# Kernel tuning notes

Hardware: AMD Instinct MI355X
Metric: run time of the kernel (lower is better)

The kernel has to match this reference:

```python
import jax, jax.numpy as jnp
import numpy as np
import math

B, S, H, NH, NKV, HD = 1, 2048, 4096, 32, 8, 128
ROPE_THETA = 10000.0


def setup_inputs() -> dict:
    key = jax.random.key(0)
    ks = jax.random.split(key, 16)
    hidden_states = jax.random.normal(ks[0], (B, S, H), jnp.float32) * 0.02
    Wq = jax.random.normal(ks[1], (NH * HD, H), jnp.float32) * 0.02
    Wk = jax.random.normal(ks[2], (NKV * HD, H), jnp.float32) * 0.02
    Wv = jax.random.normal(ks[3], (NKV * HD, H), jnp.float32) * 0.02
    Wo = jax.random.normal(ks[4], (H, NH * HD), jnp.float32) * 0.02
    # RoPE cos/sin, HF Llama convention: emb = concat(freqs, freqs)
    inv_freq = 1.0 / (ROPE_THETA ** (jnp.arange(0, HD, 2, dtype=jnp.float32) / HD))
    pos = jnp.arange(S, dtype=jnp.float32)
    freqs = pos[:, None] * inv_freq[None, :]              # [S, HD/2]
    emb = jnp.concatenate([freqs, freqs], axis=-1)        # [S, HD]
    cos = jnp.cos(emb)[None]                              # [1, S, HD]
    sin = jnp.sin(emb)[None]
    # additive causal mask [B, 1, S, S]
    causal = jnp.tril(jnp.ones((S, S), dtype=bool))
    attention_mask = jnp.where(causal, 0.0, -1e9).astype(jnp.float32)[None, None]
    # reorder permutations (as written by GPTQ act-order reordering)
    perm = lambda k, n: jax.random.permutation(k, n).astype(jnp.int32)
    return {
        'hidden_states': hidden_states, 'Wq': Wq, 'Wk': Wk, 'Wv': Wv, 'Wo': Wo,
        'cos': cos, 'sin': sin, 'attention_mask': attention_mask,
        'q_order_col': perm(ks[5], H), 'q_order_row': perm(ks[6], NH * HD),
        'k_order_col': perm(ks[7], H), 'k_order_row': perm(ks[8], NKV * HD),
        'v_order_col': perm(ks[9], H), 'v_order_row': perm(ks[10], NKV * HD),
        'o_order_col': perm(ks[11], NH * HD), 'o_order_row': perm(ks[12], H),
    }


def _rotate_half(x):
    x1, x2 = jnp.split(x, 2, axis=-1)
    return jnp.concatenate([-x2, x1], axis=-1)


def reference(hidden_states, Wq, Wk, Wv, Wo, cos, sin, attention_mask,
              q_order_col, q_order_row, k_order_col, k_order_row,
              v_order_col, v_order_row, o_order_col, o_order_row):
    bsz, q_len, _ = hidden_states.shape
    # permuted projections: gather cols of input, GEMM, gather rows of output
    q = hidden_states[:, :, q_order_col] @ Wq.T
    q = q[:, :, q_order_row]
    k = hidden_states[:, :, k_order_col] @ Wk.T
    k = k[:, :, k_order_row]
    v = hidden_states[:, :, v_order_col] @ Wv.T
    v = v[:, :, v_order_row]
    q = q.reshape(bsz, q_len, NH, HD).transpose(0, 2, 1, 3)   # [B,NH,S,HD]
    k = k.reshape(bsz, q_len, NKV, HD).transpose(0, 2, 1, 3)  # [B,NKV,S,HD]
    v = v.reshape(bsz, q_len, NKV, HD).transpose(0, 2, 1, 3)
    # RoPE
    c = cos[:, None, :, :]  # [1,1,S,HD]
    s = sin[:, None, :, :]
    q = q * c + _rotate_half(q) * s
    k = k * c + _rotate_half(k) * s
    # repeat_kv for GQA
    rep = NH // NKV
    k = jnp.repeat(k, rep, axis=1)  # [B,NH,S,HD]
    v = jnp.repeat(v, rep, axis=1)
    # eager attention: full score matrix, fp32 softmax
    scores = jnp.einsum('bhqd,bhkd->bhqk', q, k) / math.sqrt(HD)
    scores = scores + attention_mask
    probs = jax.nn.softmax(scores.astype(jnp.float32), axis=-1).astype(q.dtype)
    # dropout p=0.0 (eval) -> identity
    attn = jnp.einsum('bhqk,bhkd->bhqd', probs, v)
    attn = attn.transpose(0, 2, 1, 3).reshape(bsz, q_len, NH * HD)
    out = attn[:, :, o_order_col] @ Wo.T
    out = out[:, :, o_order_row]
    return out
```

## Files before the change

kernel.cpp:

```cpp
#include <hip/hip_runtime.h>

typedef unsigned short u16;
typedef unsigned char u8;
typedef __bf16 bf16x8 __attribute__((ext_vector_type(8)));
typedef float f32x4 __attribute__((ext_vector_type(4)));
typedef int i32x4 __attribute__((ext_vector_type(4)));
typedef int i32x8 __attribute__((ext_vector_type(8)));

__device__ __forceinline__ u16 f2bf(float f) {
    unsigned u = __float_as_uint(f);
    unsigned r = (u + 0x7fffu + ((u >> 16) & 1u)) >> 16;
    return (u16)r;
}
__device__ __forceinline__ float bf2f(u16 h) {
    return __uint_as_float(((unsigned)h) << 16);
}
__device__ __forceinline__ unsigned pack_bf2(float lo, float hi) {
    unsigned a = __float_as_uint(hi) + 0x8000u;
    unsigned b = __float_as_uint(lo) + 0x8000u;
    return __builtin_amdgcn_perm(a, b, 0x07060302u);
}
__device__ __forceinline__ unsigned pack_fp8x4(float a, float b, float c, float d) {
    unsigned w = __builtin_amdgcn_cvt_pk_fp8_f32(a, b, 0, false);
    w = __builtin_amdgcn_cvt_pk_fp8_f32(c, d, w, true);
    return w;
}
__device__ __forceinline__ void async_copy16(const void* g, void* l) {
    __builtin_amdgcn_global_load_lds((__attribute__((address_space(1))) void*)(void*)g,
                                     (__attribute__((address_space(3))) void*)l, 16, 0, 0);
}

#define FP8_SCALE 64.0f
#define FP8_UNSCALE (1.0f / 4096.0f)


__global__ void inv4_k(const int* __restrict__ q, const int* __restrict__ k,
                       const int* __restrict__ v, const int* __restrict__ o,
                       int* __restrict__ invq, int* __restrict__ invk,
                       int* __restrict__ invv, int* __restrict__ invo) {
    int i = blockIdx.x * 256 + threadIdx.x;
    int a = i >> 12, j = i & 4095;
    const int* p = a == 0 ? q : a == 1 ? k : a == 2 ? v : o;
    int* inv = a == 0 ? invq : a == 1 ? invk : a == 2 ? invv : invo;
    inv[p[j]] = j;
}

__global__ __launch_bounds__(256) void permw4_k(
    const float* __restrict__ Wq, const float* __restrict__ Wk,
    const float* __restrict__ Wv, const float* __restrict__ Wo,
    const int* __restrict__ qor, const int* __restrict__ kor,
    const int* __restrict__ vor, const int* __restrict__ oor,
    const int* __restrict__ invq, const int* __restrict__ invk,
    const int* __restrict__ invv, const int* __restrict__ invo,
    u8* __restrict__ Wqkf8, u16* __restrict__ Wvp, u16* __restrict__ Wop) {
    __shared__ float rowbuf[4096];
    int j = blockIdx.x;
    const float* W; const int* rp; const int* inv; int row; int f8;
    u8* out8 = nullptr; u16* out16 = nullptr;
    if (j < 4096)      { W = Wq; rp = qor; inv = invq; row = j;        out8 = Wqkf8 + (size_t)j * 4096; f8 = 1; }
    else if (j < 5120) { W = Wk; rp = kor; inv = invk; row = j - 4096; out8 = Wqkf8 + (size_t)j * 4096; f8 = 1; }
    else if (j < 6144) { W = Wv; rp = vor; inv = invv; row = j - 5120; out16 = Wvp + (size_t)(j - 5120) * 4096; f8 = 0; }
    else               { W = Wo; rp = oor; inv = invo; row = j - 6144; out16 = Wop + (size_t)(j - 6144) * 4096; f8 = 0; }
    if (f8) {
        int hd = row & 127, b = hd >> 4;
        row = (row & ~127) | ((hd & 15) | ((b & 1) << 6) | ((b & 2) << 3) | ((hd & 64) >> 1));
    }
    const float4* wr4 = (const float4*)(W + (size_t)rp[row] * 4096);
#pragma unroll
    for (int t = 0; t < 4; t++)
        ((float4*)rowbuf)[threadIdx.x + t * 256] = wr4[threadIdx.x + t * 256];
    __syncthreads();
    if (f8) {
        int t = threadIdx.x;
        const int4* inv4p = (const int4*)inv;
        float v[16];
#pragma unroll
        for (int u = 0; u < 4; u++) {
            int4 ix = inv4p[t * 4 + u];
            v[4 * u + 0] = rowbuf[ix.x] * FP8_SCALE;
            v[4 * u + 1] = rowbuf[ix.y] * FP8_SCALE;
            v[4 * u + 2] = rowbuf[ix.z] * FP8_SCALE;
            v[4 * u + 3] = rowbuf[ix.w] * FP8_SCALE;
        }
        uint4 wv;
        wv.x = pack_fp8x4(v[0], v[1], v[2], v[3]);
        wv.y = pack_fp8x4(v[4], v[5], v[6], v[7]);
        wv.z = pack_fp8x4(v[8], v[9], v[10], v[11]);
        wv.w = pack_fp8x4(v[12], v[13], v[14], v[15]);
        int tb = (t & ~7) | ((t & 7) ^ (j & 7));
        ((uint4*)out8)[tb] = wv;
    } else {
        unsigned* o32 = (unsigned*)out16;
        const int2* inv2 = (const int2*)inv;
#pragma unroll
        for (int t = 0; t < 8; t++) {
            int c = threadIdx.x + t * 256;
            int2 ij = inv2[c];
            o32[c] = pack_bf2(rowbuf[ij.x], rowbuf[ij.y]);
        }
    }
}

__global__ __launch_bounds__(256) void cvt_k(const float* __restrict__ x,
                                             u16* __restrict__ Xb,
                                             u8* __restrict__ Xf8) {
    int row = blockIdx.x;
    int t = threadIdx.x;
    const float4* src = (const float4*)(x + (size_t)row * 4096);
    float v[16];
#pragma unroll
    for (int u = 0; u < 4; u++) {
        float4 a = src[t * 4 + u];
        v[4 * u + 0] = a.x; v[4 * u + 1] = a.y; v[4 * u + 2] = a.z; v[4 * u + 3] = a.w;
    }
    uint4 b0, b1;
    b0.x = pack_bf2(v[0], v[1]);  b0.y = pack_bf2(v[2], v[3]);
    b0.z = pack_bf2(v[4], v[5]);  b0.w = pack_bf2(v[6], v[7]);
    b1.x = pack_bf2(v[8], v[9]);  b1.y = pack_bf2(v[10], v[11]);
    b1.z = pack_bf2(v[12], v[13]); b1.w = pack_bf2(v[14], v[15]);
    uint4* ob = (uint4*)(Xb + (size_t)row * 4096);
    ob[t * 2] = b0;
    ob[t * 2 + 1] = b1;
    uint4 w8;
    w8.x = pack_fp8x4(v[0] * FP8_SCALE, v[1] * FP8_SCALE, v[2] * FP8_SCALE, v[3] * FP8_SCALE);
    w8.y = pack_fp8x4(v[4] * FP8_SCALE, v[5] * FP8_SCALE, v[6] * FP8_SCALE, v[7] * FP8_SCALE);
    w8.z = pack_fp8x4(v[8] * FP8_SCALE, v[9] * FP8_SCALE, v[10] * FP8_SCALE, v[11] * FP8_SCALE);
    w8.w = pack_fp8x4(v[12] * FP8_SCALE, v[13] * FP8_SCALE, v[14] * FP8_SCALE, v[15] * FP8_SCALE);
    int tb = (t & ~7) | ((t & 7) ^ (row & 7));
    ((uint4*)(Xf8 + (size_t)row * 4096))[tb] = w8;
}

__global__ __launch_bounds__(256) void vtr_k(const float* __restrict__ Vpart,
                                             u16* __restrict__ Vt) {
    __shared__ u16 t[64][65];
    int bx = blockIdx.x;
    int s0 = (bx & 31) * 64, c0 = (bx >> 5) * 64;
    int x = threadIdx.x & 63, y4 = threadIdx.x >> 6;
    const float* Vp0 = Vpart;
    const float* Vp1 = Vpart + (size_t)2048 * 1024;
    for (int i = 0; i < 16; i++) {
        int r = y4 * 16 + i;
        size_t idx = (size_t)(s0 + r) * 1024 + c0 + x;
        t[r][x] = f2bf(Vp0[idx] + Vp1[idx]);
    }
    __syncthreads();
    for (int i = 0; i < 16; i++) {
        int r = y4 * 16 + i;
        int xk = 4 * (x & 15) + (x >> 4);
        Vt[(size_t)(c0 + r) * 2048 + s0 + xk] = t[x][r];
    }
}


#define QKV_BAR() asm volatile("s_barrier" ::: "memory")

#define QK_STAGE(bufi, kt) do {                                                   \
    u8* d_ = S8 + (bufi) * 32768 + tid * 16;                                      \
    const int k0_ = (kt) * 128;                                                   \
    async_copy16(AgQ + k0_, d_);                                                  \
    async_copy16(AgQ + (size_t)64 * 4096 + k0_, d_ + 8192);                       \
    async_copy16(BgQ + k0_, d_ + 16384);                                          \
    async_copy16(BgQ + (size_t)64 * 4096 + k0_, d_ + 24576);                      \
} while (0)

#define QK_COMPUTE(bufi) do {                                                     \
    const u8* la_ = S8 + (bufi) * 32768;                                          \
    const u8* lb_ = la_ + 16384;                                                  \
    i32x8 af0, af1, bf0, bf1;                                                     \
    union { i32x8 v8; i32x4 v4[2]; } u_;                                          \
    int R_ = (wn + l16) * 128;                                                    \
    u_.v4[0] = *(const i32x4*)&lb_[R_ + s0b];                                     \
    u_.v4[1] = *(const i32x4*)&lb_[R_ + s1b]; bf0 = u_.v8;                        \
    R_ = (wn + 16 + l16) * 128;                                                   \
    u_.v4[0] = *(const i32x4*)&lb_[R_ + s0b];                                     \
    u_.v4[1] = *(const i32x4*)&lb_[R_ + s1b]; bf1 = u_.v8;                        \
    R_ = (wm + l16) * 128;                                                        \
    u_.v4[0] = *(const i32x4*)&la_[R_ + s0b];                                     \
    u_.v4[1] = *(const i32x4*)&la_[R_ + s1b]; af0 = u_.v8;                        \
    R_ = (wm + 16 + l16) * 128;                                                   \
    u_.v4[0] = *(const i32x4*)&la_[R_ + s0b];                                     \
    u_.v4[1] = *(const i32x4*)&la_[R_ + s1b]; af1 = u_.v8;                        \
    asm volatile("s_waitcnt lgkmcnt(0)" ::: "memory");                            \
    __builtin_amdgcn_sched_barrier(0);                                            \
    __builtin_amdgcn_s_setprio(1);                                                \
    acc[0][0] = __builtin_amdgcn_mfma_scale_f32_16x16x128_f8f6f4(af0, bf0, acc[0][0], 0, 0, 0, 0x7F7F7F7F, 0, 0x7F7F7F7F); \
    acc[0][1] = __builtin_amdgcn_mfma_scale_f32_16x16x128_f8f6f4(af0, bf1, acc[0][1], 0, 0, 0, 0x7F7F7F7F, 0, 0x7F7F7F7F); \
    acc[1][0] = __builtin_amdgcn_mfma_scale_f32_16x16x128_f8f6f4(af1, bf0, acc[1][0], 0, 0, 0, 0x7F7F7F7F, 0, 0x7F7F7F7F); \
    acc[1][1] = __builtin_amdgcn_mfma_scale_f32_16x16x128_f8f6f4(af1, bf1, acc[1][1], 0, 0, 0, 0x7F7F7F7F, 0, 0x7F7F7F7F); \
    __builtin_amdgcn_s_setprio(0);                                                \
    R_ = (wm + 32 + l16) * 128;                                                   \
    u_.v4[0] = *(const i32x4*)&la_[R_ + s0b];                                     \
    u_.v4[1] = *(const i32x4*)&la_[R_ + s1b]; af0 = u_.v8;                        \
    R_ = (wm + 48 + l16) * 128;                                                   \
    u_.v4[0] = *(const i32x4*)&la_[R_ + s0b];                                     \
    u_.v4[1] = *(const i32x4*)&la_[R_ + s1b]; af1 = u_.v8;                        \
    asm volatile("s_waitcnt lgkmcnt(0)" ::: "memory");                            \
    __builtin_amdgcn_sched_barrier(0);                                            \
    __builtin_amdgcn_s_setprio(1);                                                \
    acc[2][0] = __builtin_amdgcn_mfma_scale_f32_16x16x128_f8f6f4(af0, bf0, acc[2][0], 0, 0, 0, 0x7F7F7F7F, 0, 0x7F7F7F7F); \
    acc[2][1] = __builtin_amdgcn_mfma_scale_f32_16x16x128_f8f6f4(af0, bf1, acc[2][1], 0, 0, 0, 0x7F7F7F7F, 0, 0x7F7F7F7F); \
    acc[3][0] = __builtin_amdgcn_mfma_scale_f32_16x16x128_f8f6f4(af1, bf0, acc[3][0], 0, 0, 0, 0x7F7F7F7F, 0, 0x7F7F7F7F); \
    acc[3][1] = __builtin_amdgcn_mfma_scale_f32_16x16x128_f8f6f4(af1, bf1, acc[3][1], 0, 0, 0, 0x7F7F7F7F, 0, 0x7F7F7F7F); \
    __builtin_amdgcn_s_setprio(0);                                                \
} while (0)

#define V_STAGE(bufi, kt) do {                                                    \
    u8* d_ = S8 + (bufi) * 32768 + tid * 16;                                      \
    const int k0_ = (kt) * 64;                                                    \
    async_copy16(AgV + k0_, d_);                                                  \
    async_copy16(AgV + (size_t)64 * 4096 + k0_, d_ + 8192);                       \
    async_copy16(BgV + k0_, d_ + 16384);                                          \
    async_copy16(BgV + (size_t)64 * 4096 + k0_, d_ + 24576);                      \
} while (0)

#define V_COMPUTE(bufi) do {                                                      \
    const u16* la_ = (const u16*)(S8 + (bufi) * 32768);                           \
    const u16* lb_ = la_ + 8192;                                                  \
    _Pragma("unroll")                                                             \
    for (int kk_ = 0; kk_ < 2; kk_++) {                                           \
        const int so_ = ((kk_ * 4 + quad) ^ swz) * 8;                             \
        bf16x8 bv0 = *(const bf16x8*)&lb_[(wn + l16) * 64 + so_];                 \
        bf16x8 bv1 = *(const bf16x8*)&lb_[(wn + 16 + l16) * 64 + so_];            \
        bf16x8 a0 = *(const bf16x8*)&la_[(wm + l16) * 64 + so_];                  \
        bf16x8 a1 = *(const bf16x8*)&la_[(wm + 16 + l16) * 64 + so_];             \
        bf16x8 a2 = *(const bf16x8*)&la_[(wm + 32 + l16) * 64 + so_];             \
        bf16x8 a3 = *(const bf16x8*)&la_[(wm + 48 + l16) * 64 + so_];             \
        asm volatile("s_waitcnt lgkmcnt(0)" ::: "memory");                        \
        __builtin_amdgcn_sched_barrier(0);                                        \
        __builtin_amdgcn_s_setprio(1);                                            \
        acc[0][0] = __builtin_amdgcn_mfma_f32_16x16x32_bf16(a0, bv0, acc[0][0], 0, 0, 0); \
        acc[0][1] = __builtin_amdgcn_mfma_f32_16x16x32_bf16(a0, bv1, acc[0][1], 0, 0, 0); \
        acc[1][0] = __builtin_amdgcn_mfma_f32_16x16x32_bf16(a1, bv0, acc[1][0], 0, 0, 0); \
        acc[1][1] = __builtin_amdgcn_mfma_f32_16x16x32_bf16(a1, bv1, acc[1][1], 0, 0, 0); \
        acc[2][0] = __builtin_amdgcn_mfma_f32_16x16x32_bf16(a2, bv0, acc[2][0], 0, 0, 0); \
        acc[2][1] = __builtin_amdgcn_mfma_f32_16x16x32_bf16(a2, bv1, acc[2][1], 0, 0, 0); \
        acc[3][0] = __builtin_amdgcn_mfma_f32_16x16x32_bf16(a3, bv0, acc[3][0], 0, 0, 0); \
        acc[3][1] = __builtin_amdgcn_mfma_f32_16x16x32_bf16(a3, bv1, acc[3][1], 0, 0, 0); \
        __builtin_amdgcn_s_setprio(0);                                            \
    }                                                                             \
} while (0)

__global__ __launch_bounds__(512, 2) void gemm_qkv_k(const u8* __restrict__ Xf8,
                                                     const u16* __restrict__ Xb,
                                                     const u8* __restrict__ Wqk,
                                                     const u16* __restrict__ Wv,
                                                     u16* __restrict__ QKV,
                                                     float* __restrict__ Vpart,
                                                     const float* __restrict__ cosv,
                                                     const float* __restrict__ sinv) {
    extern __shared__ u8 S8[];
    const int tid = threadIdx.x;
    const int w = tid >> 6, lane = tid & 63;
    const int quad = lane >> 4, l16 = lane & 15;
    const int bm0 = blockIdx.y * 128;
    const int wm = (w >> 2) * 64;
    const int wn = (w & 3) * 32;
    const int swz = l16 & 7;
    const int s0b = ((quad * 2) ^ swz) * 16;
    const int s1b = ((quad * 2 + 1) ^ swz) * 16;

    if (blockIdx.x < 40) {
        const int bn0 = blockIdx.x * 128;
        const u8* AgQ = Xf8 + (size_t)(bm0 + (tid >> 3)) * 4096 + (tid & 7) * 16;
        const u8* BgQ = Wqk + (size_t)(bn0 + (tid >> 3)) * 4096 + (tid & 7) * 16;
        f32x4 acc[4][2] = {};

        QK_STAGE(0, 0);
        QK_STAGE(1, 1);
        QK_STAGE(2, 2);
        asm volatile("s_waitcnt vmcnt(8)" ::: "memory");
        QKV_BAR();
        int cur = 0;
        for (int t = 0; t < 29; ++t) {
            QK_COMPUTE(cur);
            QKV_BAR();
            QK_STAGE(cur, t + 3);
            asm volatile("s_waitcnt vmcnt(8)" ::: "memory");
            QKV_BAR();
            cur = (cur == 2) ? 0 : cur + 1;
        }
        QK_COMPUTE(2);
        asm volatile("s_waitcnt vmcnt(4)" ::: "memory");
        QKV_BAR();
        QK_COMPUTE(0);
        asm volatile("s_waitcnt vmcnt(0)" ::: "memory");
        QKV_BAR();
        QK_COMPUTE(1);

        const float qsc = (bn0 < 4096) ? 0.08838834764831845f : 1.0f;
        const int d1 = (w & 3) * 16 + l16;
        const int col0 = bn0 + wn + l16;
#pragma unroll
        for (int i = 0; i < 4; i++) {
            const int row = bm0 + wm + i * 16 + quad * 4;
#pragma unroll
            for (int r = 0; r < 4; r++) {
                const int s = row + r;
                const float c  = cosv[s * 128 + d1];
                const float sn = sinv[s * 128 + d1];
                const float x1 = acc[i][0][r] * FP8_UNSCALE;
                const float x2 = acc[i][1][r] * FP8_UNSCALE;
                QKV[(size_t)s * 6144 + col0]      = f2bf((x1 * c - x2 * sn) * qsc);
                QKV[(size_t)s * 6144 + col0 + 16] = f2bf((x2 * c + x1 * sn) * qsc);
            }
        }
    } else {
        const int vx = blockIdx.x - 40;
        const int bn0 = (vx & 7) * 128;
        const int kslice = vx >> 3;
        const int kb = kslice * 2048;
        const int srow = tid >> 3;
        const int sblk = (tid & 7) ^ (srow & 7);
        const u16* AgV = Xb + (size_t)(bm0 + srow) * 4096 + kb + sblk * 8;
        const u16* BgV = Wv + (size_t)(bn0 + srow) * 4096 + kb + sblk * 8;
        f32x4 acc[4][2] = {};

        V_STAGE(0, 0);
        V_STAGE(1, 1);
        V_STAGE(2, 2);
        asm volatile("s_waitcnt vmcnt(8)" ::: "memory");
        QKV_BAR();
        int cur = 0;
        for (int t = 0; t < 29; ++t) {
            V_COMPUTE(cur);
            QKV_BAR();
            V_STAGE(cur, t + 3);
            asm volatile("s_waitcnt vmcnt(8)" ::: "memory");
            QKV_BAR();
            cur = (cur == 2) ? 0 : cur + 1;
        }
        V_COMPUTE(2);
        asm volatile("s_waitcnt vmcnt(4)" ::: "memory");
        QKV_BAR();
        V_COMPUTE(0);
        asm volatile("s_waitcnt vmcnt(0)" ::: "memory");
        QKV_BAR();
        V_COMPUTE(1);

        float* Vp = Vpart + (size_t)kslice * 2048 * 1024;
#pragma unroll
        for (int i = 0; i < 4; i++) {
            const int row = bm0 + wm + i * 16 + quad * 4;
#pragma unroll
            for (int j = 0; j < 2; j++) {
                const int col = bn0 + wn + j * 16 + l16;
#pragma unroll
                for (int r = 0; r < 4; r++)
                    Vp[(size_t)(row + r) * 1024 + col] = acc[i][j][r];
            }
        }
    }
}


#define GO_STAGE(bufi, kt) do {                                                   \
    u16* la_ = S + (bufi) * 24576;                                                \
    u16* lb_ = la_ + 16384;                                                       \
    const int k0_ = (kt) * 64;                                                    \
    _Pragma("unroll")                                                             \
    for (int u = 0; u < 4; u++)                                                   \
        async_copy16(Asrc + (size_t)u * 64 * 4096 + k0_, la_ + u * 4096 + sdst);  \
    _Pragma("unroll")                                                             \
    for (int u = 0; u < 2; u++)                                                   \
        async_copy16(Bsrc + (size_t)u * 64 * 4096 + k0_, lb_ + u * 4096 + sdst);  \
} while (0)

#define GO_COMPUTE(bufi) do {                                                     \
    const u16* la_ = S + (bufi) * 24576;                                          \
    const u16* lb_ = la_ + 16384;                                                 \
    bf16x8 bfr[4][2], afr[2][2];                                                  \
    _Pragma("unroll")                                                             \
    for (int j = 0; j < 4; j++) {                                                 \
        const int rb_ = (wn + j * 16 + l16) * 64;                                 \
        bfr[j][0] = *(const bf16x8*)&lb_[rb_ + o0];                               \
        bfr[j][1] = *(const bf16x8*)&lb_[rb_ + o1];                               \
    }                                                                             \
    _Pragma("unroll")                                                             \
    for (int i = 0; i < 2; i++) {                                                 \
        const int ra_ = (wm + i * 16 + l16) * 64;                                 \
        afr[i][0] = *(const bf16x8*)&la_[ra_ + o0];                               \
        afr[i][1] = *(const bf16x8*)&la_[ra_ + o1];                               \
    }                                                                             \
    asm volatile("s_waitcnt lgkmcnt(0)" ::: "memory");                            \
    __builtin_amdgcn_sched_barrier(0);                                            \
    __builtin_amdgcn_s_setprio(1);                                                \
    _Pragma("unroll")                                                             \
    for (int i = 0; i < 2; i++)                                                   \
        _Pragma("unroll")                                                         \
        for (int j = 0; j < 4; j++) {                                             \
            acc[i][j] = __builtin_amdgcn_mfma_f32_16x16x32_bf16(afr[i][0], bfr[j][0], acc[i][j], 0, 0, 0); \
            acc[i][j] = __builtin_amdgcn_mfma_f32_16x16x32_bf16(afr[i][1], bfr[j][1], acc[i][j], 0, 0, 0); \
        }                                                                         \
    __builtin_amdgcn_s_setprio(0);                                                \
    _Pragma("unroll")                                                             \
    for (int i = 0; i < 2; i++) {                                                 \
        const int ra_ = (wm + (i + 2) * 16 + l16) * 64;                           \
        afr[i][0] = *(const bf16x8*)&la_[ra_ + o0];                               \
        afr[i][1] = *(const bf16x8*)&la_[ra_ + o1];                               \
    }                                                                             \
    asm volatile("s_waitcnt lgkmcnt(0)" ::: "memory");                            \
    __builtin_amdgcn_sched_barrier(0);                                            \
    __builtin_amdgcn_s_setprio(1);                                                \
    _Pragma("unroll")                                                             \
    for (int i = 0; i < 2; i++)                                                   \
        _Pragma("unroll")                                                         \
        for (int j = 0; j < 4; j++) {                                             \
            acc[i + 2][j] = __builtin_amdgcn_mfma_f32_16x16x32_bf16(afr[i][0], bfr[j][0], acc[i + 2][j], 0, 0, 0); \
            acc[i + 2][j] = __builtin_amdgcn_mfma_f32_16x16x32_bf16(afr[i][1], bfr[j][1], acc[i + 2][j], 0, 0, 0); \
        }                                                                         \
    __builtin_amdgcn_s_setprio(0);                                                \
} while (0)

#define GO_BAR() asm volatile("s_barrier" ::: "memory")

__global__ __launch_bounds__(512, 2) void gemm_o_k(const u16* __restrict__ A,
                                                   const u16* __restrict__ B,
                                                   float* __restrict__ Out) {
    extern __shared__ u16 S[];
    const int tid = threadIdx.x;
    const int w = tid >> 6, lane = tid & 63;
    const int quad = lane >> 4, l16 = lane & 15;
    const int linear = blockIdx.y * 32 + blockIdx.x;
    const int wgid = (linear & 7) * 32 + (linear >> 3);
    const int bm0 = (wgid >> 5) * 256;
    const int bn0 = (wgid & 31) * 128;
    const int wm = (w >> 1) * 64;
    const int wn = (w & 1) * 64;
    const int sr = tid >> 3;
    const int scg = ((tid & 7) ^ (sr & 7)) * 8;
    const int sdst = tid * 8;
    const u16* Asrc = A + (size_t)(bm0 + sr) * 4096 + scg;
    const u16* Bsrc = B + (size_t)(bn0 + sr) * 4096 + scg;
    const int swz = l16 & 7;
    const int o0 = (quad ^ swz) * 8;
    const int o1 = ((4 | quad) ^ swz) * 8;

    f32x4 acc[4][4] = {};

    GO_STAGE(0, 0);
    GO_STAGE(1, 1);
    GO_STAGE(2, 2);
    asm volatile("s_waitcnt vmcnt(12)" ::: "memory");
    GO_BAR();

    int cur = 0;
    for (int t = 0; t < 61; ++t) {
        GO_COMPUTE(cur);
        GO_BAR();
        GO_STAGE(cur, t + 3);
        asm volatile("s_waitcnt vmcnt(12)" ::: "memory");
        GO_BAR();
        cur = (cur == 2) ? 0 : cur + 1;
    }
    GO_COMPUTE(1);
    asm volatile("s_waitcnt vmcnt(6)" ::: "memory");
    GO_BAR();
    GO_COMPUTE(2);
    asm volatile("s_waitcnt vmcnt(0)" ::: "memory");
    GO_BAR();
    GO_COMPUTE(0);

#pragma unroll
    for (int i = 0; i < 4; i++) {
        const int row = bm0 + wm + i * 16 + quad * 4;
#pragma unroll
        for (int j = 0; j < 4; j++) {
            const int col = bn0 + wn + j * 16 + l16;
#pragma unroll
            for (int r = 0; r < 4; r++)
                Out[(size_t)(row + r) * 4096 + col] = acc[i][j][r];
        }
    }
}


__global__ __launch_bounds__(256) void attn_k(const u16* __restrict__ Qb,
                                              const u16* __restrict__ Kb,
                                              const u16* __restrict__ Vt,
                                              u16* __restrict__ Ob,
                                              int qstride, int kstride) {
    __shared__ u16 ldsK[4 * 64 * 32];
    __shared__ u16 ldsV[2 * 128 * 32];
    __shared__ u16 ldsP[4][32 * 72];
    const int h = blockIdx.x;
    const int qt = (int)gridDim.y - 1 - (int)blockIdx.y;
    const int kvh = h >> 2;
    const int tid = threadIdx.x;
    const int w = tid >> 6, lane = tid & 63;
    const int quad = lane >> 4, l16 = lane & 15;
    const int q0 = qt * 128;
    const int wrow = q0 + w * 32;

    bf16x8 qf[2][4];
#pragma unroll
    for (int mi = 0; mi < 2; mi++)
#pragma unroll
        for (int kk = 0; kk < 4; kk++)
            qf[mi][kk] = *(const bf16x8*)&Qb[(size_t)(wrow + mi * 16 + l16) * qstride +
                                             h * 128 + kk * 32 + quad * 8];

    const u16* kp[4]; const u16* vp[4];
    u16* ldk[4]; u16* ldv[4];
#pragma unroll
    for (int t = 0; t < 4; t++) {
        int wl = w + t * 4;
        int kk = wl >> 2, part = wl & 3;
        kp[t] = Kb + (size_t)(part * 16 + (lane >> 2)) * kstride + kvh * 128 + kk * 32 + (lane & 3) * 8;
        int ks2 = wl >> 3, p2 = wl & 7;
        vp[t] = Vt + (size_t)(kvh * 128 + p2 * 16 + (lane >> 2)) * 2048 + ks2 * 32 + (lane & 3) * 8;
        ldk[t] = ldsK + wl * 512;
        ldv[t] = ldsV + wl * 512;
    }

    f32x4 acc_o[2][8] = {};
    float lrow[2][4] = {};

    const int nk = 2 * (qt + 1);
    for (int kn = 0; kn < nk; kn++) {
        const int g0 = kn * 64;
#pragma unroll
        for (int t = 0; t < 4; t++) async_copy16(kp[t], ldk[t]);
#pragma unroll
        for (int t = 0; t < 4; t++) async_copy16(vp[t], ldv[t]);
#pragma unroll
        for (int t = 0; t < 4; t++) { kp[t] += (size_t)64 * kstride; vp[t] += 64; }
        __syncthreads();

        if (g0 <= wrow + 31) {
            f32x4 accs[2][4] = {};
#pragma unroll
            for (int kk = 0; kk < 4; kk++) {
                bf16x8 bfrag[4];
#pragma unroll
                for (int ni = 0; ni < 4; ni++)
                    bfrag[ni] = *(const bf16x8*)&ldsK[kk * 2048 + (ni * 16 + l16) * 32 + quad * 8];
#pragma unroll
                for (int mi = 0; mi < 2; mi++)
#pragma unroll
                    for (int ni = 0; ni < 4; ni++)
                        accs[mi][ni] = __builtin_amdgcn_mfma_f32_16x16x32_bf16(
                            qf[mi][kk], bfrag[ni], accs[mi][ni], 0, 0, 0);
            }
            const bool diag = (g0 + 63 > wrow);
            int kidx[4];
#pragma unroll
            for (int ni = 0; ni < 4; ni++) kidx[ni] = g0 + ni * 16 + l16;
#pragma unroll
            for (int mi = 0; mi < 2; mi++) {
#pragma unroll
                for (int r = 0; r < 4; r++) {
                    const int qrow = wrow + mi * 16 + quad * 4 + r;
                    float p[4];
#pragma unroll
                    for (int ni = 0; ni < 4; ni++) {
                        float s = accs[mi][ni][r];
                        if (diag && (kidx[ni] > qrow)) s = -1e30f;
                        p[ni] = __expf(s);
                    }
                    lrow[mi][r] += (p[0] + p[1]) + (p[2] + p[3]);
                    uint2 pk;
                    pk.x = pack_bf2(p[0], p[1]);
                    pk.y = pack_bf2(p[2], p[3]);
                    *(uint2*)&ldsP[w][(mi * 16 + quad * 4 + r) * 72 + l16 * 4] = pk;
                }
            }
#pragma unroll
            for (int ks = 0; ks < 2; ks++) {
                bf16x8 pa[2];
#pragma unroll
                for (int mi = 0; mi < 2; mi++)
                    pa[mi] = *(const bf16x8*)&ldsP[w][(mi * 16 + l16) * 72 + ks * 32 + quad * 8];
#pragma unroll
                for (int oj = 0; oj < 8; oj++) {
                    bf16x8 vb = *(const bf16x8*)&ldsV[ks * 4096 + (oj * 16 + l16) * 32 + quad * 8];
#pragma unroll
                    for (int mi = 0; mi < 2; mi++)
                        acc_o[mi][oj] = __builtin_amdgcn_mfma_f32_16x16x32_bf16(
                            pa[mi], vb, acc_o[mi][oj], 0, 0, 0);
                }
            }
        }
        __syncthreads();
    }
#pragma unroll
    for (int mi = 0; mi < 2; mi++)
#pragma unroll
        for (int r = 0; r < 4; r++) {
            float l = lrow[mi][r];
            l += __shfl_xor(l, 1);
            l += __shfl_xor(l, 2);
            l += __shfl_xor(l, 4);
            l += __shfl_xor(l, 8);
            const float inv = 1.0f / l;
            const int qrow = wrow + mi * 16 + quad * 4 + r;
#pragma unroll
            for (int oj = 0; oj < 8; oj++)
                Ob[(size_t)qrow * 4096 + h * 128 + oj * 16 + l16] =
                    f2bf(acc_o[mi][oj][r] * inv);
        }
}


extern "C" void kernel_launch(void* const* d_in, const int* in_sizes, int n_in,
                              void* d_out, int out_size, void* d_ws, size_t ws_size,
                              hipStream_t stream) {
    (void)in_sizes; (void)n_in; (void)out_size; (void)ws_size;
    const float* hidden = (const float*)d_in[0];
    const float* Wq = (const float*)d_in[1];
    const float* Wk = (const float*)d_in[2];
    const float* Wv = (const float*)d_in[3];
    const float* Wo = (const float*)d_in[4];
    const float* cosv = (const float*)d_in[5];
    const float* sinv = (const float*)d_in[6];
    const int* qoc = (const int*)d_in[8];
    const int* qor = (const int*)d_in[9];
    const int* koc = (const int*)d_in[10];
    const int* kor = (const int*)d_in[11];
    const int* voc = (const int*)d_in[12];
    const int* vor = (const int*)d_in[13];
    const int* ooc = (const int*)d_in[14];
    const int* oor = (const int*)d_in[15];

    char* ws = (char*)d_ws;
    size_t off = 0;
    int* invq = (int*)(ws + off); off += 16384;
    int* invk = (int*)(ws + off); off += 16384;
    int* invv = (int*)(ws + off); off += 16384;
    int* invo = (int*)(ws + off); off += 16384;
    u16* Wop   = (u16*)(ws + off); off += (size_t)4096 * 4096 * 2;
    u16* Xb    = (u16*)(ws + off); off += (size_t)2048 * 4096 * 2;
    u8*  Wqkf8 = (u8*)(ws + off);  off += (size_t)5120 * 4096;
    u16* Wvp   = (u16*)(ws + off); off += (size_t)1024 * 4096 * 2;
    u8*  Xf8   = (u8*)(ws + off);  off += (size_t)2048 * 4096;
    u16* QKVb  = (u16*)(ws + off); off += (size_t)2048 * 6144 * 2;
    u16* Vtb   = (u16*)(ws + off); off += (size_t)1024 * 2048 * 2;
    float* Vpart = (float*)(ws + off); off += (size_t)2 * 2048 * 1024 * 4;
    u16* Attb  = Xb;

    inv4_k<<<64, 256, 0, stream>>>(qoc, koc, voc, ooc, invq, invk, invv, invo);
    permw4_k<<<10240, 256, 0, stream>>>(Wq, Wk, Wv, Wo, qor, kor, vor, oor,
                                        invq, invk, invv, invo, Wqkf8, Wvp, Wop);
    cvt_k<<<2048, 256, 0, stream>>>(hidden, Xb, Xf8);

    gemm_qkv_k<<<dim3(56, 16), 512, 98304, stream>>>(Xf8, Xb, Wqkf8, Wvp, QKVb, Vpart,
                                                     cosv, sinv);

    vtr_k<<<512, 256, 0, stream>>>(Vpart, Vtb);

    attn_k<<<dim3(32, 16), 256, 0, stream>>>(QKVb, QKVb + 4096, Vtb, Attb, 6144, 6144);

    gemm_o_k<<<dim3(32, 8), 512, 147456, stream>>>(Attb, Wop, (float*)d_out);
}
```

Before: 498.0 us.

## Restructure QKV GEMM to 4 waves with 64x64 warp tiles and double buffering

The QKV projection kernel drops from 8 to 4 waves per block, so each wave now computes a 64x64 output tile instead of 64x32. This raises fragment reuse from LDS and cuts LDS read traffic per MFMA. The shared-memory pipeline shrinks from triple to double buffering (64KB instead of 96KB), and the V-path LDS layout changes from swizzled rows to two 32-column halves. The attention kernel also raises wave priority around its MFMA blocks. The trade-off is fewer waves to hide latency and a shallower prefetch depth, and the unswizzled V layout may cause LDS bank conflicts.

```diff
diff --git a/kernel.cpp b/kernel.cpp
--- a/kernel.cpp
+++ b/kernel.cpp
@@ -155,92 +155,103 @@
 #define QKV_BAR() asm volatile("s_barrier" ::: "memory")
 
 #define QK_STAGE(bufi, kt) do {                                                   \
-    u8* d_ = S8 + (bufi) * 32768 + tid * 16;                                      \
+    u8* la_ = S8 + (bufi) * 32768 + w * 4096;                                     \
+    u8* lb_ = la_ + 16384;                                                        \
     const int k0_ = (kt) * 128;                                                   \
-    async_copy16(AgQ + k0_, d_);                                                  \
-    async_copy16(AgQ + (size_t)64 * 4096 + k0_, d_ + 8192);                       \
-    async_copy16(BgQ + k0_, d_ + 16384);                                          \
-    async_copy16(BgQ + (size_t)64 * 4096 + k0_, d_ + 24576);                      \
+    _Pragma("unroll")                                                             \
+    for (int t_ = 0; t_ < 4; t_++)                                                \
+        async_copy16(AgQ + (size_t)t_ * 8 * 4096 + k0_, la_ + t_ * 1024);         \
+    _Pragma("unroll")                                                             \
+    for (int t_ = 0; t_ < 4; t_++)                                                \
+        async_copy16(BgQ + (size_t)t_ * 8 * 4096 + k0_, lb_ + t_ * 1024);         \
 } while (0)
 
 #define QK_COMPUTE(bufi) do {                                                     \
     const u8* la_ = S8 + (bufi) * 32768;                                          \
     const u8* lb_ = la_ + 16384;                                                  \
-    i32x8 af0, af1, bf0, bf1;                                                     \
     union { i32x8 v8; i32x4 v4[2]; } u_;                                          \
-    int R_ = (wn + l16) * 128;                                                    \
-    u_.v4[0] = *(const i32x4*)&lb_[R_ + s0b];                                     \
-    u_.v4[1] = *(const i32x4*)&lb_[R_ + s1b]; bf0 = u_.v8;                        \
-    R_ = (wn + 16 + l16) * 128;                                                   \
-    u_.v4[0] = *(const i32x4*)&lb_[R_ + s0b];                                     \
-    u_.v4[1] = *(const i32x4*)&lb_[R_ + s1b]; bf1 = u_.v8;                        \
-    R_ = (wm + l16) * 128;                                                        \
-    u_.v4[0] = *(const i32x4*)&la_[R_ + s0b];                                     \
-    u_.v4[1] = *(const i32x4*)&la_[R_ + s1b]; af0 = u_.v8;                        \
-    R_ = (wm + 16 + l16) * 128;                                                   \
-    u_.v4[0] = *(const i32x4*)&la_[R_ + s0b];                                     \
-    u_.v4[1] = *(const i32x4*)&la_[R_ + s1b]; af1 = u_.v8;                        \
+    i32x8 bfv[4], af0, af1;                                                       \
+    _Pragma("unroll")                                                             \
+    for (int j_ = 0; j_ < 4; j_++) {                                              \
+        const int r_ = (wn + j_ * 16 + l16) * 128;                                \
+        u_.v4[0] = *(const i32x4*)&lb_[r_ + s0b];                                 \
+        u_.v4[1] = *(const i32x4*)&lb_[r_ + s1b];                                 \
+        bfv[j_] = u_.v8;                                                          \
+    }                                                                             \
+    { const int r_ = (wm + l16) * 128;                                            \
+      u_.v4[0] = *(const i32x4*)&la_[r_ + s0b];                                   \
+      u_.v4[1] = *(const i32x4*)&la_[r_ + s1b]; af0 = u_.v8; }                    \
+    { const int r_ = (wm + 16 + l16) * 128;                                       \
+      u_.v4[0] = *(const i32x4*)&la_[r_ + s0b];                                   \
+      u_.v4[1] = *(const i32x4*)&la_[r_ + s1b]; af1 = u_.v8; }                    \
     asm volatile("s_waitcnt lgkmcnt(0)" ::: "memory");                            \
     __builtin_amdgcn_sched_barrier(0);                                            \
     __builtin_amdgcn_s_setprio(1);                                                \
-    acc[0][0] = __builtin_amdgcn_mfma_scale_f32_16x16x128_f8f6f4(af0, bf0, acc[0][0], 0, 0, 0, 0x7F7F7F7F, 0, 0x7F7F7F7F); \
-    acc[0][1] = __builtin_amdgcn_mfma_scale_f32_16x16x128_f8f6f4(af0, bf1, acc[0][1], 0, 0, 0, 0x7F7F7F7F, 0, 0x7F7F7F7F); \
-    acc[1][0] = __builtin_amdgcn_mfma_scale_f32_16x16x128_f8f6f4(af1, bf0, acc[1][0], 0, 0, 0, 0x7F7F7F7F, 0, 0x7F7F7F7F); \
-    acc[1][1] = __builtin_amdgcn_mfma_scale_f32_16x16x128_f8f6f4(af1, bf1, acc[1][1], 0, 0, 0, 0x7F7F7F7F, 0, 0x7F7F7F7F); \
+    _Pragma("unroll")                                                             \
+    for (int j_ = 0; j_ < 4; j_++) {                                              \
+        acc[0][j_] = __builtin_amdgcn_mfma_scale_f32_16x16x128_f8f6f4(af0, bfv[j_], acc[0][j_], 0, 0, 0, 0x7F7F7F7F, 0, 0x7F7F7F7F); \
+        acc[1][j_] = __builtin_amdgcn_mfma_scale_f32_16x16x128_f8f6f4(af1, bfv[j_], acc[1][j_], 0, 0, 0, 0x7F7F7F7F, 0, 0x7F7F7F7F); \
+    }                                                                             \
     __builtin_amdgcn_s_setprio(0);                                                \
-    R_ = (wm + 32 + l16) * 128;                                                   \
-    u_.v4[0] = *(const i32x4*)&la_[R_ + s0b];                                     \
-    u_.v4[1] = *(const i32x4*)&la_[R_ + s1b]; af0 = u_.v8;                        \
-    R_ = (wm + 48 + l16) * 128;                                                   \
-    u_.v4[0] = *(const i32x4*)&la_[R_ + s0b];                                     \
-    u_.v4[1] = *(const i32x4*)&la_[R_ + s1b]; af1 = u_.v8;                        \
+    { const int r_ = (wm + 32 + l16) * 128;                                       \
+      u_.v4[0] = *(const i32x4*)&la_[r_ + s0b];                                   \
+      u_.v4[1] = *(const i32x4*)&la_[r_ + s1b]; af0 = u_.v8; }                    \
+    { const int r_ = (wm + 48 + l16) * 128;                                       \
+      u_.v4[0] = *(const i32x4*)&la_[r_ + s0b];                                   \
+      u_.v4[1] = *(const i32x4*)&la_[r_ + s1b]; af1 = u_.v8; }                    \
     asm volatile("s_waitcnt lgkmcnt(0)" ::: "memory");                            \
     __builtin_amdgcn_sched_barrier(0);                                            \
     __builtin_amdgcn_s_setprio(1);                                                \
-    acc[2][0] = __builtin_amdgcn_mfma_scale_f32_16x16x128_f8f6f4(af0, bf0, acc[2][0], 0, 0, 0, 0x7F7F7F7F, 0, 0x7F7F7F7F); \
-    acc[2][1] = __builtin_amdgcn_mfma_scale_f32_16x16x128_f8f6f4(af0, bf1, acc[2][1], 0, 0, 0, 0x7F7F7F7F, 0, 0x7F7F7F7F); \
-    acc[3][0] = __builtin_amdgcn_mfma_scale_f32_16x16x128_f8f6f4(af1, bf0, acc[3][0], 0, 0, 0, 0x7F7F7F7F, 0, 0x7F7F7F7F); \
-    acc[3][1] = __builtin_amdgcn_mfma_scale_f32_16x16x128_f8f6f4(af1, bf1, acc[3][1], 0, 0, 0, 0x7F7F7F7F, 0, 0x7F7F7F7F); \
+    _Pragma("unroll")                                                             \
+    for (int j_ = 0; j_ < 4; j_++) {                                              \
+        acc[2][j_] = __builtin_amdgcn_mfma_scale_f32_16x16x128_f8f6f4(af0, bfv[j_], acc[2][j_], 0, 0, 0, 0x7F7F7F7F, 0, 0x7F7F7F7F); \
+        acc[3][j_] = __builtin_amdgcn_mfma_scale_f32_16x16x128_f8f6f4(af1, bfv[j_], acc[3][j_], 0, 0, 0, 0x7F7F7F7F, 0, 0x7F7F7F7F); \
+    }                                                                             \
     __builtin_amdgcn_s_setprio(0);                                                \
 } while (0)
 
 #define V_STAGE(bufi, kt) do {                                                    \
-    u8* d_ = S8 + (bufi) * 32768 + tid * 16;                                      \
+    u16* a0_ = (u16*)(S8 + (bufi) * 32768);                                       \
+    u16* a1_ = a0_ + 4096;                                                        \
+    u16* b0_ = a0_ + 8192;                                                        \
+    u16* b1_ = a0_ + 12288;                                                       \
     const int k0_ = (kt) * 64;                                                    \
-    async_copy16(AgV + k0_, d_);                                                  \
-    async_copy16(AgV + (size_t)64 * 4096 + k0_, d_ + 8192);                       \
-    async_copy16(BgV + k0_, d_ + 16384);                                          \
-    async_copy16(BgV + (size_t)64 * 4096 + k0_, d_ + 24576);                      \
+    async_copy16(AgV + k0_,                          a0_ + w * 512);              \
+    async_copy16(AgV + (size_t)64 * 4096 + k0_,      a0_ + (w + 4) * 512);        \
+    async_copy16(AgV + k0_ + 32,                     a1_ + w * 512);              \
+    async_copy16(AgV + (size_t)64 * 4096 + k0_ + 32, a1_ + (w + 4) * 512);        \
+    async_copy16(BgV + k0_,                          b0_ + w * 512);              \
+    async_copy16(BgV + (size_t)64 * 4096 + k0_,      b0_ + (w + 4) * 512);        \
+    async_copy16(BgV + k0_ + 32,                     b1_ + w * 512);              \
+    async_copy16(BgV + (size_t)64 * 4096 + k0_ + 32, b1_ + (w + 4) * 512);        \
 } while (0)
 
 #define V_COMPUTE(bufi) do {                                                      \
-    const u16* la_ = (const u16*)(S8 + (bufi) * 32768);                           \
-    const u16* lb_ = la_ + 8192;                                                  \
+    const u16* base_ = (const u16*)(S8 + (bufi) * 32768);                         \
     _Pragma("unroll")                                                             \
     for (int kk_ = 0; kk_ < 2; kk_++) {                                           \
-        const int so_ = ((kk_ * 4 + quad) ^ swz) * 8;                             \
-        bf16x8 bv0 = *(const bf16x8*)&lb_[(wn + l16) * 64 + so_];                 \
-        bf16x8 bv1 = *(const bf16x8*)&lb_[(wn + 16 + l16) * 64 + so_];            \
-        bf16x8 a0 = *(const bf16x8*)&la_[(wm + l16) * 64 + so_];                  \
-        bf16x8 a1 = *(const bf16x8*)&la_[(wm + 16 + l16) * 64 + so_];             \
-        bf16x8 a2 = *(const bf16x8*)&la_[(wm + 32 + l16) * 64 + so_];             \
-        bf16x8 a3 = *(const bf16x8*)&la_[(wm + 48 + l16) * 64 + so_];             \
+        const u16* la_ = base_ + kk_ * 4096;                                      \
+        const u16* lb_ = base_ + 8192 + kk_ * 4096;                               \
+        bf16x8 af[4], bfv[4];                                                     \
+        _Pragma("unroll")                                                         \
+        for (int i_ = 0; i_ < 4; i_++)                                            \
+            af[i_] = *(const bf16x8*)&la_[(wm + i_ * 16 + l16) * 32 + quad * 8];  \
+        _Pragma("unroll")                                                         \
+        for (int j_ = 0; j_ < 4; j_++)                                            \
+            bfv[j_] = *(const bf16x8*)&lb_[(wn + j_ * 16 + l16) * 32 + quad * 8]; \
         asm volatile("s_waitcnt lgkmcnt(0)" ::: "memory");                        \
         __builtin_amdgcn_sched_barrier(0);                                        \
         __builtin_amdgcn_s_setprio(1);                                            \
-        acc[0][0] = __builtin_amdgcn_mfma_f32_16x16x32_bf16(a0, bv0, acc[0][0], 0, 0, 0); \
-        acc[0][1] = __builtin_amdgcn_mfma_f32_16x16x32_bf16(a0, bv1, acc[0][1], 0, 0, 0); \
-        acc[1][0] = __builtin_amdgcn_mfma_f32_16x16x32_bf16(a1, bv0, acc[1][0], 0, 0, 0); \
-        acc[1][1] = __builtin_amdgcn_mfma_f32_16x16x32_bf16(a1, bv1, acc[1][1], 0, 0, 0); \
-        acc[2][0] = __builtin_amdgcn_mfma_f32_16x16x32_bf16(a2, bv0, acc[2][0], 0, 0, 0); \
-        acc[2][1] = __builtin_amdgcn_mfma_f32_16x16x32_bf16(a2, bv1, acc[2][1], 0, 0, 0); \
-        acc[3][0] = __builtin_amdgcn_mfma_f32_16x16x32_bf16(a3, bv0, acc[3][0], 0, 0, 0); \
-        acc[3][1] = __builtin_amdgcn_mfma_f32_16x16x32_bf16(a3, bv1, acc[3][1], 0, 0, 0); \
+        _Pragma("unroll")                                                         \
+        for (int i_ = 0; i_ < 4; i_++)                                            \
+            _Pragma("unroll")                                                     \
+            for (int j_ = 0; j_ < 4; j_++)                                        \
+                acc[i_][j_] = __builtin_amdgcn_mfma_f32_16x16x32_bf16(af[i_], bfv[j_], acc[i_][j_], 0, 0, 0); \
         __builtin_amdgcn_s_setprio(0);                                            \
     }                                                                             \
 } while (0)
 
-__global__ __launch_bounds__(512, 2) void gemm_qkv_k(const u8* __restrict__ Xf8,
+__global__ __launch_bounds__(256, 2) void gemm_qkv_k(const u8* __restrict__ Xf8,
                                                      const u16* __restrict__ Xb,
                                                      const u8* __restrict__ Wqk,
                                                      const u16* __restrict__ Wv,
@@ -253,55 +264,54 @@
     const int w = tid >> 6, lane = tid & 63;
     const int quad = lane >> 4, l16 = lane & 15;
     const int bm0 = blockIdx.y * 128;
-    const int wm = (w >> 2) * 64;
-    const int wn = (w & 3) * 32;
+    const int wm = (w >> 1) * 64, wn = (w & 1) * 64;
     const int swz = l16 & 7;
     const int s0b = ((quad * 2) ^ swz) * 16;
     const int s1b = ((quad * 2 + 1) ^ swz) * 16;
 
     if (blockIdx.x < 40) {
         const int bn0 = blockIdx.x * 128;
-        const u8* AgQ = Xf8 + (size_t)(bm0 + (tid >> 3)) * 4096 + (tid & 7) * 16;
-        const u8* BgQ = Wqk + (size_t)(bn0 + (tid >> 3)) * 4096 + (tid & 7) * 16;
-        f32x4 acc[4][2] = {};
+        const u8* AgQ = Xf8 + (size_t)(bm0 + w * 32 + (lane >> 3)) * 4096 + (lane & 7) * 16;
+        const u8* BgQ = Wqk + (size_t)(bn0 + w * 32 + (lane >> 3)) * 4096 + (lane & 7) * 16;
+        f32x4 acc[4][4] = {};
 
         QK_STAGE(0, 0);
         QK_STAGE(1, 1);
-        QK_STAGE(2, 2);
         asm volatile("s_waitcnt vmcnt(8)" ::: "memory");
         QKV_BAR();
         int cur = 0;
-        for (int t = 0; t < 29; ++t) {
+        for (int t = 0; t < 30; ++t) {
             QK_COMPUTE(cur);
             QKV_BAR();
-            QK_STAGE(cur, t + 3);
+            QK_STAGE(cur, t + 2);
             asm volatile("s_waitcnt vmcnt(8)" ::: "memory");
             QKV_BAR();
-            cur = (cur == 2) ? 0 : cur + 1;
-        }
-        QK_COMPUTE(2);
-        asm volatile("s_waitcnt vmcnt(4)" ::: "memory");
-        QKV_BAR();
+            cur ^= 1;
+        }
         QK_COMPUTE(0);
         asm volatile("s_waitcnt vmcnt(0)" ::: "memory");
         QKV_BAR();
         QK_COMPUTE(1);
 
         const float qsc = (bn0 < 4096) ? 0.08838834764831845f : 1.0f;
-        const int d1 = (w & 3) * 16 + l16;
-        const int col0 = bn0 + wn + l16;
+        const int hb = (wn ? 32 : 0) + l16;
 #pragma unroll
         for (int i = 0; i < 4; i++) {
             const int row = bm0 + wm + i * 16 + quad * 4;
 #pragma unroll
-            for (int r = 0; r < 4; r++) {
-                const int s = row + r;
-                const float c  = cosv[s * 128 + d1];
-                const float sn = sinv[s * 128 + d1];
-                const float x1 = acc[i][0][r] * FP8_UNSCALE;
-                const float x2 = acc[i][1][r] * FP8_UNSCALE;
-                QKV[(size_t)s * 6144 + col0]      = f2bf((x1 * c - x2 * sn) * qsc);
-                QKV[(size_t)s * 6144 + col0 + 16] = f2bf((x2 * c + x1 * sn) * qsc);
+            for (int jp = 0; jp < 2; jp++) {
+                const int d1 = hb + jp * 16;
+                const int ce = bn0 + wn + jp * 32 + l16;
+#pragma unroll
+                for (int r = 0; r < 4; r++) {
+                    const int s = row + r;
+                    const float c  = cosv[s * 128 + d1];
+                    const float sn = sinv[s * 128 + d1];
+                    const float x1 = acc[i][jp * 2][r]     * FP8_UNSCALE;
+                    const float x2 = acc[i][jp * 2 + 1][r] * FP8_UNSCALE;
+                    QKV[(size_t)s * 6144 + ce]      = f2bf((x1 * c - x2 * sn) * qsc);
+                    QKV[(size_t)s * 6144 + ce + 16] = f2bf((x2 * c + x1 * sn) * qsc);
+                }
             }
         }
     } else {
@@ -309,29 +319,25 @@
         const int bn0 = (vx & 7) * 128;
         const int kslice = vx >> 3;
         const int kb = kslice * 2048;
-        const int srow = tid >> 3;
-        const int sblk = (tid & 7) ^ (srow & 7);
-        const u16* AgV = Xb + (size_t)(bm0 + srow) * 4096 + kb + sblk * 8;
-        const u16* BgV = Wv + (size_t)(bn0 + srow) * 4096 + kb + sblk * 8;
-        f32x4 acc[4][2] = {};
+        const int r0 = w * 16 + (lane >> 2);
+        const int c0 = (lane & 3) * 8;
+        const u16* AgV = Xb + (size_t)(bm0 + r0) * 4096 + kb + c0;
+        const u16* BgV = Wv + (size_t)(bn0 + r0) * 4096 + kb + c0;
+        f32x4 acc[4][4] = {};
 
         V_STAGE(0, 0);
         V_STAGE(1, 1);
-        V_STAGE(2, 2);
         asm volatile("s_waitcnt vmcnt(8)" ::: "memory");
         QKV_BAR();
         int cur = 0;
-        for (int t = 0; t < 29; ++t) {
+        for (int t = 0; t < 30; ++t) {
             V_COMPUTE(cur);
             QKV_BAR();
-            V_STAGE(cur, t + 3);
+            V_STAGE(cur, t + 2);
             asm volatile("s_waitcnt vmcnt(8)" ::: "memory");
             QKV_BAR();
-            cur = (cur == 2) ? 0 : cur + 1;
-        }
-        V_COMPUTE(2);
-        asm volatile("s_waitcnt vmcnt(4)" ::: "memory");
-        QKV_BAR();
+            cur ^= 1;
+        }
         V_COMPUTE(0);
         asm volatile("s_waitcnt vmcnt(0)" ::: "memory");
         QKV_BAR();
@@ -342,7 +348,7 @@
         for (int i = 0; i < 4; i++) {
             const int row = bm0 + wm + i * 16 + quad * 4;
 #pragma unroll
-            for (int j = 0; j < 2; j++) {
+            for (int j = 0; j < 4; j++) {
                 const int col = bn0 + wn + j * 16 + l16;
 #pragma unroll
                 for (int r = 0; r < 4; r++)
@@ -534,12 +540,14 @@
 #pragma unroll
                 for (int ni = 0; ni < 4; ni++)
                     bfrag[ni] = *(const bf16x8*)&ldsK[kk * 2048 + (ni * 16 + l16) * 32 + quad * 8];
+                __builtin_amdgcn_s_setprio(1);
 #pragma unroll
                 for (int mi = 0; mi < 2; mi++)
 #pragma unroll
                     for (int ni = 0; ni < 4; ni++)
                         accs[mi][ni] = __builtin_amdgcn_mfma_f32_16x16x32_bf16(
                             qf[mi][kk], bfrag[ni], accs[mi][ni], 0, 0, 0);
+                __builtin_amdgcn_s_setprio(0);
             }
             const bool diag = (g0 + 63 > wrow);
             int kidx[4];
@@ -570,6 +578,7 @@
 #pragma unroll
                 for (int mi = 0; mi < 2; mi++)
                     pa[mi] = *(const bf16x8*)&ldsP[w][(mi * 16 + l16) * 72 + ks * 32 + quad * 8];
+                __builtin_amdgcn_s_setprio(1);
 #pragma unroll
                 for (int oj = 0; oj < 8; oj++) {
                     bf16x8 vb = *(const bf16x8*)&ldsV[ks * 4096 + (oj * 16 + l16) * 32 + quad * 8];
@@ -578,6 +587,7 @@
                         acc_o[mi][oj] = __builtin_amdgcn_mfma_f32_16x16x32_bf16(
                             pa[mi], vb, acc_o[mi][oj], 0, 0, 0);
                 }
+                __builtin_amdgcn_s_setprio(0);
             }
         }
         __syncthreads();
@@ -642,7 +652,7 @@
                                         invq, invk, invv, invo, Wqkf8, Wvp, Wop);
     cvt_k<<<2048, 256, 0, stream>>>(hidden, Xb, Xf8);
 
-    gemm_qkv_k<<<dim3(56, 16), 512, 98304, stream>>>(Xf8, Xb, Wqkf8, Wvp, QKVb, Vpart,
+    gemm_qkv_k<<<dim3(56, 16), 256, 65536, stream>>>(Xf8, Xb, Wqkf8, Wvp, QKVb, Vpart,
                                                      cosv, sinv);
 
     vtr_k<<<512, 256, 0, stream>>>(Vpart, Vtb);
```

After: 471.7 us. 5.3% less time.
